# Kernel optimization log

Hardware: AMD Instinct MI355X
Metric: run time of the kernel (lower is better)

## Reference

```python
import jax, jax.numpy as jnp
import numpy as np

NU, NS, NM = 80000, 20000, 30000
D = 128
E_UI, E_MM = 1_500_000, 480_000
B, L = 2048, 32
LAYERS = 2


def spmm(rows, cols, vals, x, n):
    # sparse [n,n] @ dense [n,d] via gather + segment_sum
    return jax.ops.segment_sum(vals[:, None] * x[cols], rows, num_segments=n)


def setup_inputs() -> dict:
    key = jax.random.key(0)
    ks = jax.random.split(key, 20)
    inp = {}
    inp['mashup_inputs'] = jax.random.randint(ks[0], (B,), 0, NM, dtype=jnp.int32)
    inp['service_inputs'] = jax.random.randint(ks[1], (B,), 0, NS, dtype=jnp.int32)
    inp['member_masked'] = jax.random.randint(ks[2], (B, L), 0, NU, dtype=jnp.int32)
    # variable-length compose lists: length in [1, L]; mask==1 marks padding
    lens = jax.random.randint(ks[3], (B, 1), 1, L + 1)
    inp['mask'] = (jnp.arange(L)[None, :] >= lens).astype(jnp.float32)
    inp['member_masked'] = jnp.where(inp['mask'] > 0, 0, inp['member_masked'])
    inp['adj_rows'] = jax.random.randint(ks[4], (E_UI,), 0, NU + NS, dtype=jnp.int32)
    inp['adj_cols'] = jax.random.randint(ks[5], (E_UI,), 0, NU + NS, dtype=jnp.int32)
    inp['adj_vals'] = jax.random.uniform(ks[6], (E_UI,)) * 0.1
    inp['A_rows'] = jax.random.randint(ks[7], (E_MM,), 0, NM, dtype=jnp.int32)
    inp['A_cols'] = jax.random.randint(ks[8], (E_MM,), 0, NM, dtype=jnp.int32)
    inp['A_vals'] = jax.random.uniform(ks[9], (E_MM,)) * 0.1
    inp['d_inv'] = jax.random.uniform(ks[10], (NM,)) * 0.1
    s = 0.05
    inp['user_tbl'] = jax.random.normal(ks[11], (NU, D)) * s
    inp['service_tbl'] = jax.random.normal(ks[12], (NS, D)) * s
    inp['mashup_tbl'] = jax.random.normal(ks[13], (NM, D)) * s
    inp['att_w1'] = jax.random.normal(ks[14], (2 * D, 16)) * s
    inp['att_b1'] = jnp.zeros((16,))
    inp['att_w2'] = jax.random.normal(ks[15], (16, 1)) * s
    inp['att_b2'] = jnp.zeros((1,))
    inp['pred_w1'] = jax.random.normal(ks[16], (3 * D, 8)) * s
    inp['pred_b1'] = jnp.zeros((8,))
    inp['pred_w2'] = jax.random.normal(ks[17], (8, 1)) * s
    inp['pred_b2'] = jnp.zeros((1,))
    return inp


def reference(mashup_inputs, service_inputs, member_masked, adj_rows, adj_cols,
              A_rows, A_cols, mask, user_tbl, service_tbl, mashup_tbl,
              adj_vals, A_vals, d_inv, att_w1, att_b1, att_w2, att_b2,
              pred_w1, pred_b1, pred_w2, pred_b2):
    # HyperConv on concatenated user+service embeddings (layer-mean aggregation)
    ui = jnp.concatenate([user_tbl, service_tbl], axis=0)  # [NU+NS, D]
    acc, h = ui, ui
    for _ in range(LAYERS):
        h = spmm(adj_rows, adj_cols, adj_vals, h, NU + NS)
        acc = acc + h
    ui = acc / (LAYERS + 1)
    user_e, service_e = ui[:NU], ui[NU:]
    service_emb = service_e[service_inputs]  # [B, D]

    # HyperConv2 on mashup graph: emb <- D^-1 A emb per layer, layer-mean
    acc, m = mashup_tbl, mashup_tbl
    for _ in range(LAYERS):
        m = d_inv[:, None] * spmm(A_rows, A_cols, A_vals, m, NM)
        acc = acc + m
    mashup_embedding = acc / (LAYERS + 1)

    # ragged gather + masked attention pooling over compose members
    member_emb = user_e[member_masked]                      # [B, L, D]
    svc_exp = jnp.broadcast_to(service_emb[:, None, :], (B, L, D))
    at_emb = jnp.concatenate([member_emb, svc_exp], axis=2)  # [B, L, 2D]
    hdn = jax.nn.relu(at_emb @ att_w1 + att_b1)             # [B, L, 16]
    scores = (hdn @ att_w2 + att_b2)[..., 0]                 # [B, L]
    scores = jnp.where(mask > 0, -1e9, scores)               # mask padding
    at_wt = jax.nn.softmax(scores, axis=1)
    g_att = jnp.einsum('bl,bld->bd', at_wt, member_emb)      # [B, D]

    mashup_emb = g_att + mashup_embedding[mashup_inputs]
    elem = mashup_emb * service_emb
    new_emb = jnp.concatenate([elem, mashup_emb, service_emb], axis=1)  # [B, 3D]
    hp = jax.nn.relu(new_emb @ pred_w1 + pred_b1)
    y = jax.nn.sigmoid(hp @ pred_w2 + pred_b2)               # [B, 1]
    return y
```

## Files before the change

kernel.cpp:

```cpp
#include <hip/hip_runtime.h>
#include <climits>

#define NU_ 80000
#define NS_ 20000
#define NM_ 30000
#define UIN_ (NU_ + NS_)
#define DD 128
#define LL 32
#define RPB 64
#define NCH 256
#define NBUK_UI ((UIN_ + RPB - 1) / RPB)
#define NBUK_MM ((NM_  + RPB - 1) / RPB)

#define F8_SCALE 512.0f
#define F8_INV   (1.0f / 512.0f)

typedef unsigned int   uint32;
typedef unsigned short ushort_t;
typedef unsigned char  uchar_t;
typedef float f32x2 __attribute__((ext_vector_type(2)));

__device__ __forceinline__ float bflo(uint32 u) { return __uint_as_float(u << 16); }
__device__ __forceinline__ float bfhi(uint32 u) { return __uint_as_float(u & 0xffff0000u); }
__device__ __forceinline__ uint32 f2bf(float f) {
    uint32 u = __float_as_uint(f);
    return (u + 0x7fffu + ((u >> 16) & 1u)) >> 16;
}
__device__ __forceinline__ uint32 pack2bf(float lo, float hi) {
    return f2bf(lo) | (f2bf(hi) << 16);
}

__device__ __forceinline__ float dec1_f8(uint32 b) {
    uint32 em = b & 0x7fu;
    uint32 s  = (b & 0x80u) << 24;
    float vn = __uint_as_float(s | (((em >> 3) + 120u) << 23) | ((em & 7u) << 20));
    float vd = (float)(int)em * 0.001953125f;
    vd = (b & 0x80u) ? -vd : vd;
    return (em >= 8u) ? vn : vd;
}
__device__ __forceinline__ uint32 enc1_f8(float f) {
    uint32 u = __float_as_uint(f);
    uint32 s = (u >> 31) << 7;
    float a = fabsf(f);
    if (a >= 448.0f) return s | 0x7Eu;
    if (a < 0.015625f) {
        int m = (int)(a * 512.0f + 0.5f);
        return s | (uint32)m;
    }
    uint32 au = u & 0x7fffffffu;
    au += 0x7FFFFu + ((au >> 20) & 1u);
    uint32 em = (((au >> 23) - 120u) << 3) | ((au >> 20) & 7u);
    if (em >= 0x7Fu) em = 0x7Eu;
    return s | em;
}
__device__ __forceinline__ f32x2 dec2_f8(uint32 u) {
#if __has_builtin(__builtin_amdgcn_cvt_pk_f32_fp8)
    return __builtin_amdgcn_cvt_pk_f32_fp8(u, false);
#else
    f32x2 r; r.x = dec1_f8(u & 0xffu); r.y = dec1_f8((u >> 8) & 0xffu); return r;
#endif
}
__device__ __forceinline__ f32x2 dec2_f8_hi(uint32 u) {
#if __has_builtin(__builtin_amdgcn_cvt_pk_f32_fp8)
    return __builtin_amdgcn_cvt_pk_f32_fp8(u, true);
#else
    f32x2 r; r.x = dec1_f8((u >> 16) & 0xffu); r.y = dec1_f8(u >> 24); return r;
#endif
}
__device__ __forceinline__ uint32 pack2f8(float lo, float hi) {
#if __has_builtin(__builtin_amdgcn_cvt_pk_fp8_f32)
    return (uint32)__builtin_amdgcn_cvt_pk_fp8_f32(lo, hi, 0, false) & 0xFFFFu;
#else
    return enc1_f8(lo) | (enc1_f8(hi) << 8);
#endif
}

__global__ void convert_fused(const float* __restrict__ user_tbl,
                              const float* __restrict__ service_tbl,
                              const float* __restrict__ mashup_tbl,
                              uint32* __restrict__ ui_bf, ushort_t* __restrict__ ui_f8,
                              uint32* __restrict__ mash_bf, ushort_t* __restrict__ mash_f8) {
    const size_t P_UI = (size_t)UIN_ * 64;
    const size_t P_MM = (size_t)NM_ * 64;
    const size_t SPLIT = (size_t)NU_ * DD;
    size_t stride = (size_t)gridDim.x * blockDim.x;
    for (size_t i = (size_t)blockIdx.x * blockDim.x + threadIdx.x; i < P_UI + P_MM; i += stride) {
        if (i < P_UI) {
            size_t e = i * 2;
            const float* s = (e < SPLIT) ? (user_tbl + e) : (service_tbl + (e - SPLIT));
            float2 v = *reinterpret_cast<const float2*>(s);
            ui_bf[i] = pack2bf(v.x, v.y);
            ui_f8[i] = (ushort_t)pack2f8(v.x * F8_SCALE, v.y * F8_SCALE);
        } else {
            size_t j = i - P_UI;
            float2 v = *reinterpret_cast<const float2*>(mashup_tbl + j * 2);
            mash_bf[j] = pack2bf(v.x, v.y);
            mash_f8[j] = (ushort_t)pack2f8(v.x * F8_SCALE, v.y * F8_SCALE);
        }
    }
}

__global__ __launch_bounds__(1024) void hist_fused(
    const int* __restrict__ rows_ui, int E_ui, int csz_ui, int* __restrict__ h_ui,
    const int* __restrict__ rows_mm, int E_mm, int csz_mm, int* __restrict__ h_mm) {
    __shared__ int hist[NBUK_UI];
    const int* rows; int E, csz, nbuk, c; int* h;
    if ((int)blockIdx.x < NCH) { rows = rows_ui; E = E_ui; csz = csz_ui; h = h_ui; nbuk = NBUK_UI; c = blockIdx.x; }
    else                       { rows = rows_mm; E = E_mm; csz = csz_mm; h = h_mm; nbuk = NBUK_MM; c = blockIdx.x - NCH; }
    for (int i = threadIdx.x; i < nbuk; i += 1024) hist[i] = 0;
    __syncthreads();
    const int lo = c * csz, hi = min(lo + csz, E);
    int i = lo + threadIdx.x;
    for (; i + 3 * 1024 < hi; i += 4 * 1024) {
        int r0 = rows[i];
        int r1 = rows[i + 1024];
        int r2 = rows[i + 2048];
        int r3 = rows[i + 3072];
        atomicAdd(&hist[r0 >> 6], 1);
        atomicAdd(&hist[r1 >> 6], 1);
        atomicAdd(&hist[r2 >> 6], 1);
        atomicAdd(&hist[r3 >> 6], 1);
    }
    for (; i < hi; i += 1024) atomicAdd(&hist[rows[i] >> 6], 1);
    __syncthreads();
    for (int b = threadIdx.x; b < nbuk; b += 1024)
        h[b * NCH + c] = hist[b];
}

__global__ __launch_bounds__(256) void scan_blocksum_fused(
    const int* __restrict__ h_ui, int n_ui, int* __restrict__ bs_ui, int nb_ui,
    const int* __restrict__ h_mm, int n_mm, int* __restrict__ bs_mm) {
    __shared__ int red[256];
    const int* cnt; int n, b; int* bsum;
    if ((int)blockIdx.x < nb_ui) { cnt = h_ui; n = n_ui; bsum = bs_ui; b = blockIdx.x; }
    else                         { cnt = h_mm; n = n_mm; bsum = bs_mm; b = blockIdx.x - nb_ui; }
    int base = b * 1024 + threadIdx.x * 4;
    int s = 0;
    if (base + 3 < n) {
        int4 v = *reinterpret_cast<const int4*>(cnt + base);
        s = v.x + v.y + v.z + v.w;
    } else {
        for (int i = base; i < n && i < base + 4; ++i) s += cnt[i];
    }
    red[threadIdx.x] = s;
    __syncthreads();
    for (int off = 128; off >= 1; off >>= 1) {
        if (threadIdx.x < off) red[threadIdx.x] += red[threadIdx.x + off];
        __syncthreads();
    }
    if (threadIdx.x == 0) bsum[b] = red[0];
}

__global__ __launch_bounds__(256) void scan_final_fused(
    int* __restrict__ h_ui, int n_ui, const int* __restrict__ bs_ui, int nb_ui,
    int* __restrict__ s_ui,
    int* __restrict__ h_mm, int n_mm, const int* __restrict__ bs_mm,
    int* __restrict__ s_mm) {
    __shared__ int lds[256];
    __shared__ int blk_off_s;
    const int tid = threadIdx.x;
    int* cnt; int n, b; const int* bsum; int* row_ptr;
    if ((int)blockIdx.x < nb_ui) { cnt = h_ui; n = n_ui; bsum = bs_ui; row_ptr = s_ui; b = blockIdx.x; }
    else                         { cnt = h_mm; n = n_mm; bsum = bs_mm; row_ptr = s_mm; b = blockIdx.x - nb_ui; }

    int s = 0;
    for (int j = tid; j < b; j += 256) s += bsum[j];
    lds[tid] = s;
    __syncthreads();
    for (int off = 128; off >= 1; off >>= 1) {
        if (tid < off) lds[tid] += lds[tid + off];
        __syncthreads();
    }
    if (tid == 0) blk_off_s = lds[0];
    __syncthreads();
    const int blk_off = blk_off_s;

    int base = b * 1024 + tid * 4;
    int c0 = 0, c1 = 0, c2 = 0, c3 = 0;
    if (base + 3 < n) {
        int4 v = *reinterpret_cast<const int4*>(cnt + base);
        c0 = v.x; c1 = v.y; c2 = v.z; c3 = v.w;
    } else {
        if (base     < n) c0 = cnt[base];
        if (base + 1 < n) c1 = cnt[base + 1];
        if (base + 2 < n) c2 = cnt[base + 2];
        if (base + 3 < n) c3 = cnt[base + 3];
    }
    int tsum = c0 + c1 + c2 + c3;
    __syncthreads();
    lds[tid] = tsum;
    __syncthreads();
    for (int off = 1; off < 256; off <<= 1) {
        int v = (tid >= off) ? lds[tid - off] : 0;
        __syncthreads();
        lds[tid] += v;
        __syncthreads();
    }
    int p0 = blk_off + ((tid > 0) ? lds[tid - 1] : 0);
    int p1 = p0 + c0, p2 = p1 + c1, p3 = p2 + c2, p4 = p3 + c3;

    if (base     < n) { row_ptr[base]     = p0; if (base     == n - 1) row_ptr[n] = p1; }
    if (base + 1 < n) { row_ptr[base + 1] = p1; if (base + 1 == n - 1) row_ptr[n] = p2; }
    if (base + 2 < n) { row_ptr[base + 2] = p2; if (base + 2 == n - 1) row_ptr[n] = p3; }
    if (base + 3 < n) { row_ptr[base + 3] = p3; if (base + 3 == n - 1) row_ptr[n] = p4; }
}

__global__ __launch_bounds__(1024) void scatter_fused(
    const int* __restrict__ rows_ui, const int* __restrict__ cols_ui,
    const float* __restrict__ vals_ui, const int* __restrict__ s_ui,
    int E_ui, int csz_ui, uint2* __restrict__ cvA_ui,
    const int* __restrict__ rows_mm, const int* __restrict__ cols_mm,
    const float* __restrict__ vals_mm, const int* __restrict__ s_mm,
    int E_mm, int csz_mm, uint2* __restrict__ cvA_mm) {
    __shared__ int cur[NBUK_UI];
    const int *rows, *cols; const float* vals; const int* s;
    int E, csz, nbuk, c; uint2* cvA;
    if ((int)blockIdx.x < NCH) {
        rows = rows_ui; cols = cols_ui; vals = vals_ui; s = s_ui;
        E = E_ui; csz = csz_ui; nbuk = NBUK_UI; c = blockIdx.x; cvA = cvA_ui;
    } else {
        rows = rows_mm; cols = cols_mm; vals = vals_mm; s = s_mm;
        E = E_mm; csz = csz_mm; nbuk = NBUK_MM; c = blockIdx.x - NCH; cvA = cvA_mm;
    }
    for (int b = threadIdx.x; b < nbuk; b += 1024) cur[b] = s[b * NCH + c];
    __syncthreads();
    const int lo = c * csz, hi = min(lo + csz, E);
    int i = lo + threadIdx.x;
    for (; i + 3 * 1024 < hi; i += 4 * 1024) {
        int   r0 = rows[i],        r1 = rows[i + 1024];
        int   r2 = rows[i + 2048], r3 = rows[i + 3072];
        int   q0 = cols[i],        q1 = cols[i + 1024];
        int   q2 = cols[i + 2048], q3 = cols[i + 3072];
        float v0 = vals[i],        v1 = vals[i + 1024];
        float v2 = vals[i + 2048], v3 = vals[i + 3072];
        int p0 = atomicAdd(&cur[r0 >> 6], 1);
        int p1 = atomicAdd(&cur[r1 >> 6], 1);
        int p2 = atomicAdd(&cur[r2 >> 6], 1);
        int p3 = atomicAdd(&cur[r3 >> 6], 1);
        cvA[p0] = make_uint2((uint32)q0 | ((uint32)(r0 & 63) << 25), __float_as_uint(v0));
        cvA[p1] = make_uint2((uint32)q1 | ((uint32)(r1 & 63) << 25), __float_as_uint(v1));
        cvA[p2] = make_uint2((uint32)q2 | ((uint32)(r2 & 63) << 25), __float_as_uint(v2));
        cvA[p3] = make_uint2((uint32)q3 | ((uint32)(r3 & 63) << 25), __float_as_uint(v3));
    }
    for (; i < hi; i += 1024) {
        int r = rows[i];
        int pos = atomicAdd(&cur[r >> 6], 1);
        cvA[pos] = make_uint2((uint32)cols[i] | ((uint32)(r & 63) << 25),
                              __float_as_uint(vals[i]));
    }
}

__device__ __forceinline__ void sort_one_bucket(
    const uint2* __restrict__ cvA, const int* __restrict__ s,
    uint2* __restrict__ cvB, int* __restrict__ row_ptr, int nrows, int b,
    int* cnt, int* cur) {
    const int tid  = threadIdx.x;
    const int base = s[b * NCH];
    const int endb = s[(b + 1) * NCH];

    if (tid < RPB) cnt[tid] = 0;
    __syncthreads();
    for (int i = base + tid; i < endb; i += 256)
        atomicAdd(&cnt[cvA[i].x >> 25], 1);
    __syncthreads();
    if (tid < 64) {
        int c = cnt[tid];
        int x = c;
        #pragma unroll
        for (int off = 1; off < 64; off <<= 1) {
            int v = __shfl_up(x, off);
            if (tid >= off) x += v;
        }
        int excl = base + x - c;
        cur[tid] = excl;
        int grow = b * RPB + tid;
        if (grow <= nrows) row_ptr[grow] = excl;
    }
    __syncthreads();
    for (int i = base + tid; i < endb; i += 256) {
        uint2 e = cvA[i];
        int rl  = (int)(e.x >> 25);
        int pos = atomicAdd(&cur[rl], 1);
        cvB[pos] = make_uint2(e.x & 0x1FFFFFFu, e.y);
    }
}

__global__ __launch_bounds__(256) void sort_fused(
    const uint2* __restrict__ cvA_ui, const int* __restrict__ s_ui,
    uint2* __restrict__ cvB_ui, int* __restrict__ rp_ui,
    const uint2* __restrict__ cvA_mm, const int* __restrict__ s_mm,
    uint2* __restrict__ cvB_mm, int* __restrict__ rp_mm) {
    __shared__ int cnt[RPB];
    __shared__ int cur[RPB];
    if ((int)blockIdx.x < NBUK_UI)
        sort_one_bucket(cvA_ui, s_ui, cvB_ui, rp_ui, UIN_, blockIdx.x, cnt, cur);
    else
        sort_one_bucket(cvA_mm, s_mm, cvB_mm, rp_mm, NM_, blockIdx.x - NBUK_UI, cnt, cur);
}

template <int MODE>
__device__ __forceinline__ void pull_row(
    const int wid, const int lane,
    const int* __restrict__ row_ptr, const uint2* __restrict__ cv,
    const uchar_t* __restrict__ x, const float* __restrict__ d_inv,
    const uint32* __restrict__ orig_bf, const uchar_t* __restrict__ hprev_f8,
    void* __restrict__ out)
{
    const int q    = lane >> 4;
    const int ql   = lane & 15;
    const int beg  = row_ptr[wid];
    const int end  = row_ptr[wid + 1];
    const int boff = ql << 3;

    float a0 = 0.f, a1 = 0.f, a2 = 0.f, a3 = 0.f;
    float a4 = 0.f, a5 = 0.f, a6 = 0.f, a7 = 0.f;

    int e = beg + q;
    for (; e + 12 < end; e += 16) {
        uint2 p0 = cv[e],     p1 = cv[e + 4];
        uint2 p2 = cv[e + 8], p3 = cv[e + 12];
        uint2 g0 = *reinterpret_cast<const uint2*>(x + (((size_t)p0.x) << 7) + boff);
        uint2 g1 = *reinterpret_cast<const uint2*>(x + (((size_t)p1.x) << 7) + boff);
        uint2 g2 = *reinterpret_cast<const uint2*>(x + (((size_t)p2.x) << 7) + boff);
        uint2 g3 = *reinterpret_cast<const uint2*>(x + (((size_t)p3.x) << 7) + boff);
        float v0 = __uint_as_float(p0.y), v1 = __uint_as_float(p1.y);
        float v2 = __uint_as_float(p2.y), v3 = __uint_as_float(p3.y);
        {
            f32x2 d0 = dec2_f8(g0.x), d1 = dec2_f8_hi(g0.x);
            f32x2 d2 = dec2_f8(g0.y), d3 = dec2_f8_hi(g0.y);
            a0 += v0 * d0.x; a1 += v0 * d0.y; a2 += v0 * d1.x; a3 += v0 * d1.y;
            a4 += v0 * d2.x; a5 += v0 * d2.y; a6 += v0 * d3.x; a7 += v0 * d3.y;
        }
        {
            f32x2 d0 = dec2_f8(g1.x), d1 = dec2_f8_hi(g1.x);
            f32x2 d2 = dec2_f8(g1.y), d3 = dec2_f8_hi(g1.y);
            a0 += v1 * d0.x; a1 += v1 * d0.y; a2 += v1 * d1.x; a3 += v1 * d1.y;
            a4 += v1 * d2.x; a5 += v1 * d2.y; a6 += v1 * d3.x; a7 += v1 * d3.y;
        }
        {
            f32x2 d0 = dec2_f8(g2.x), d1 = dec2_f8_hi(g2.x);
            f32x2 d2 = dec2_f8(g2.y), d3 = dec2_f8_hi(g2.y);
            a0 += v2 * d0.x; a1 += v2 * d0.y; a2 += v2 * d1.x; a3 += v2 * d1.y;
            a4 += v2 * d2.x; a5 += v2 * d2.y; a6 += v2 * d3.x; a7 += v2 * d3.y;
        }
        {
            f32x2 d0 = dec2_f8(g3.x), d1 = dec2_f8_hi(g3.x);
            f32x2 d2 = dec2_f8(g3.y), d3 = dec2_f8_hi(g3.y);
            a0 += v3 * d0.x; a1 += v3 * d0.y; a2 += v3 * d1.x; a3 += v3 * d1.y;
            a4 += v3 * d2.x; a5 += v3 * d2.y; a6 += v3 * d3.x; a7 += v3 * d3.y;
        }
    }
    for (; e < end; e += 4) {
        uint2 pa = cv[e];
        uint2 ga = *reinterpret_cast<const uint2*>(x + (((size_t)pa.x) << 7) + boff);
        float va = __uint_as_float(pa.y);
        f32x2 d0 = dec2_f8(ga.x), d1 = dec2_f8_hi(ga.x);
        f32x2 d2 = dec2_f8(ga.y), d3 = dec2_f8_hi(ga.y);
        a0 += va * d0.x; a1 += va * d0.y; a2 += va * d1.x; a3 += va * d1.y;
        a4 += va * d2.x; a5 += va * d2.y; a6 += va * d3.x; a7 += va * d3.y;
    }

    a0 += __shfl_xor(a0, 16); a0 += __shfl_xor(a0, 32);
    a1 += __shfl_xor(a1, 16); a1 += __shfl_xor(a1, 32);
    a2 += __shfl_xor(a2, 16); a2 += __shfl_xor(a2, 32);
    a3 += __shfl_xor(a3, 16); a3 += __shfl_xor(a3, 32);
    a4 += __shfl_xor(a4, 16); a4 += __shfl_xor(a4, 32);
    a5 += __shfl_xor(a5, 16); a5 += __shfl_xor(a5, 32);
    a6 += __shfl_xor(a6, 16); a6 += __shfl_xor(a6, 32);
    a7 += __shfl_xor(a7, 16); a7 += __shfl_xor(a7, 32);

    if (lane < 16) {
        if (MODE & 1) {
            float s = d_inv[wid];
            a0 *= s; a1 *= s; a2 *= s; a3 *= s;
            a4 *= s; a5 *= s; a6 *= s; a7 *= s;
        }
        if (MODE & 2) {
            const float inv3 = 1.0f / 3.0f;
            uint4 o = *reinterpret_cast<const uint4*>(orig_bf + (size_t)wid * 64 + (ql << 2));
            uint2 hp = *reinterpret_cast<const uint2*>(hprev_f8 + (((size_t)wid) << 7) + boff);
            f32x2 h0 = dec2_f8(hp.x), h1 = dec2_f8_hi(hp.x);
            f32x2 h2 = dec2_f8(hp.y), h3 = dec2_f8_hi(hp.y);
            uint4 r;
            r.x = pack2bf((bflo(o.x) + (h0.x + a0) * F8_INV) * inv3,
                          (bfhi(o.x) + (h0.y + a1) * F8_INV) * inv3);
            r.y = pack2bf((bflo(o.y) + (h1.x + a2) * F8_INV) * inv3,
                          (bfhi(o.y) + (h1.y + a3) * F8_INV) * inv3);
            r.z = pack2bf((bflo(o.z) + (h2.x + a4) * F8_INV) * inv3,
                          (bfhi(o.z) + (h2.y + a5) * F8_INV) * inv3);
            r.w = pack2bf((bflo(o.w) + (h3.x + a6) * F8_INV) * inv3,
                          (bfhi(o.w) + (h3.y + a7) * F8_INV) * inv3);
            *reinterpret_cast<uint4*>(reinterpret_cast<uint32*>(out) + (size_t)wid * 64 + (ql << 2)) = r;
        } else {
            uint2 r;
            r.x = pack2f8(a0, a1) | (pack2f8(a2, a3) << 16);
            r.y = pack2f8(a4, a5) | (pack2f8(a6, a7) << 16);
            *reinterpret_cast<uint2*>((uchar_t*)out + (((size_t)wid) << 7) + boff) = r;
        }
    }
}

__global__ __launch_bounds__(256) void pull_L1_fused(
    const int* __restrict__ rp_ui, const uint2* __restrict__ cv_ui,
    const uchar_t* __restrict__ x_ui, uchar_t* __restrict__ out_ui,
    const int* __restrict__ rp_mm, const uint2* __restrict__ cv_mm,
    const uchar_t* __restrict__ x_mm, const float* __restrict__ d_inv,
    uchar_t* __restrict__ out_mm, int ui_blocks)
{
    const int lane = threadIdx.x & 63;
    const int w    = threadIdx.x >> 6;
    if ((int)blockIdx.x < ui_blocks) {
        int wid = blockIdx.x * 4 + w;
        if (wid < UIN_)
            pull_row<0>(wid, lane, rp_ui, cv_ui, x_ui, nullptr, nullptr, nullptr, out_ui);
    } else {
        int wid = (blockIdx.x - ui_blocks) * 4 + w;
        if (wid < NM_)
            pull_row<1>(wid, lane, rp_mm, cv_mm, x_mm, d_inv, nullptr, nullptr, out_mm);
    }
}

__global__ __launch_bounds__(256) void pull_L2_fused(
    const int* __restrict__ rp_ui, const uint2* __restrict__ cv_ui,
    const uchar_t* __restrict__ h1_f8, const uint32* __restrict__ ui_bf,
    uint32* __restrict__ h2,
    const int* __restrict__ rp_mm, const uint2* __restrict__ cv_mm,
    const uchar_t* __restrict__ m1_f8, const float* __restrict__ d_inv,
    const uint32* __restrict__ mash_bf, uint32* __restrict__ m2, int ui_blocks)
{
    const int lane = threadIdx.x & 63;
    const int w    = threadIdx.x >> 6;
    if ((int)blockIdx.x < ui_blocks) {
        int wid = blockIdx.x * 4 + w;
        if (wid < UIN_)
            pull_row<2>(wid, lane, rp_ui, cv_ui, h1_f8, nullptr, ui_bf, h1_f8, h2);
    } else {
        int wid = (blockIdx.x - ui_blocks) * 4 + w;
        if (wid < NM_)
            pull_row<3>(wid, lane, rp_mm, cv_mm, m1_f8, d_inv, mash_bf, m1_f8, m2);
    }
}

__global__ __launch_bounds__(512) void attn_pred_kernel(
    const int* __restrict__ mashup_inputs, const int* __restrict__ service_inputs,
    const int* __restrict__ member_masked, const float* __restrict__ mask,
    const uint32* __restrict__ ui_final, const uint32* __restrict__ mash_final,
    const float* __restrict__ att_w1, const float* __restrict__ att_b1,
    const float* __restrict__ att_w2, const float* __restrict__ att_b2,
    const float* __restrict__ pred_w1, const float* __restrict__ pred_b1,
    const float* __restrict__ pred_w2, const float* __restrict__ pred_b2,
    float* __restrict__ out)
{
    const int b   = blockIdx.x;
    const int tid = threadIdx.x;

    __shared__ float mem_lds[LL * 129];
    __shared__ float svc_lds[DD];
    __shared__ float mash_lds[DD];
    __shared__ float w1_lds[2 * DD * 16];
    __shared__ float hdnw_lds[LL * 16];
    __shared__ float wt_lds[LL];
    __shared__ float new_lds[3 * DD];
    __shared__ float hp_lds[8];
    __shared__ int   midx[LL];

    if (tid < LL) midx[tid] = member_masked[b * LL + tid];
    for (int i = tid; i < 2 * DD * 16; i += 512) w1_lds[i] = att_w1[i];
    if (tid < 64) {
        int sidx = service_inputs[b];
        uint32 u = ui_final[(size_t)(NU_ + sidx) * 64 + tid];
        svc_lds[tid * 2]     = bflo(u);
        svc_lds[tid * 2 + 1] = bfhi(u);
    } else if (tid >= 448) {
        int t  = tid - 448;
        int mi = mashup_inputs[b];
        uint32 u = mash_final[(size_t)mi * 64 + t];
        mash_lds[t * 2]     = bflo(u);
        mash_lds[t * 2 + 1] = bfhi(u);
    }
    __syncthreads();

    for (int i = tid; i < LL * 64; i += 512) {
        int l = i >> 6, dp = (i & 63) * 2;
        uint32 u = ui_final[(size_t)midx[l] * 64 + (i & 63)];
        mem_lds[l * 129 + dp]     = bflo(u);
        mem_lds[l * 129 + dp + 1] = bfhi(u);
    }
    __syncthreads();

    {
        int l = tid >> 4, j = tid & 15;
        float acc = att_b1[j];
        const float* m = &mem_lds[l * 129];
        #pragma unroll 4
        for (int k = 0; k < DD; ++k) acc += m[k] * w1_lds[k * 16 + j];
        #pragma unroll 4
        for (int k = 0; k < DD; ++k) acc += svc_lds[k] * w1_lds[(DD + k) * 16 + j];
        acc = fmaxf(acc, 0.0f);
        hdnw_lds[l * 16 + j] = acc * att_w2[j];
    }
    __syncthreads();

    if (tid < 64) {
        float s = -3.0e38f;
        if (tid < LL) {
            s = att_b2[0];
            for (int j = 0; j < 16; ++j) s += hdnw_lds[tid * 16 + j];
            if (mask[b * LL + tid] > 0.0f) s = -1.0e9f;
        }
        float mx = s;
        for (int off = 16; off >= 1; off >>= 1) mx = fmaxf(mx, __shfl_xor(mx, off));
        float ex = (tid < LL) ? __expf(s - mx) : 0.0f;
        float sum = ex;
        for (int off = 16; off >= 1; off >>= 1) sum += __shfl_xor(sum, off);
        if (tid < LL) wt_lds[tid] = ex / sum;
    }
    __syncthreads();

    if (tid < DD) {
        float g = 0.0f;
        #pragma unroll 4
        for (int l = 0; l < LL; ++l) g += wt_lds[l] * mem_lds[l * 129 + tid];
        float me = g + mash_lds[tid];
        float sv = svc_lds[tid];
        new_lds[tid]          = me * sv;
        new_lds[DD + tid]     = me;
        new_lds[2 * DD + tid] = sv;
    }
    __syncthreads();

    if (tid < 8) {
        float acc = pred_b1[tid];
        for (int k = 0; k < 3 * DD; ++k) acc += new_lds[k] * pred_w1[k * 8 + tid];
        acc = fmaxf(acc, 0.0f);
        hp_lds[tid] = acc * pred_w2[tid];
    }
    __syncthreads();

    if (tid == 0) {
        float z = pred_b2[0];
        for (int j = 0; j < 8; ++j) z += hp_lds[j];
        out[b] = 1.0f / (1.0f + __expf(-z));
    }
}

extern "C" void kernel_launch(void* const* d_in, const int* in_sizes, int n_in,
                              void* d_out, int out_size, void* d_ws, size_t ws_size,
                              hipStream_t stream) {
    const int*   mashup_inputs  = (const int*)  d_in[0];
    const int*   service_inputs = (const int*)  d_in[1];
    const int*   member_masked  = (const int*)  d_in[2];
    const float* mask           = (const float*)d_in[3];
    const int*   adj_rows       = (const int*)  d_in[4];
    const int*   adj_cols       = (const int*)  d_in[5];
    const float* adj_vals       = (const float*)d_in[6];
    const int*   A_rows         = (const int*)  d_in[7];
    const int*   A_cols         = (const int*)  d_in[8];
    const float* A_vals         = (const float*)d_in[9];
    const float* d_inv          = (const float*)d_in[10];
    const float* user_tbl       = (const float*)d_in[11];
    const float* service_tbl    = (const float*)d_in[12];
    const float* mashup_tbl     = (const float*)d_in[13];
    const float* att_w1         = (const float*)d_in[14];
    const float* att_b1         = (const float*)d_in[15];
    const float* att_w2         = (const float*)d_in[16];
    const float* att_b2         = (const float*)d_in[17];
    const float* pred_w1        = (const float*)d_in[18];
    const float* pred_b1        = (const float*)d_in[19];
    const float* pred_w2        = (const float*)d_in[20];
    const float* pred_b2        = (const float*)d_in[21];

    const int E_ui = in_sizes[4];
    const int E_mm = in_sizes[7];
    const int B    = in_sizes[0];

    const int N_UI2  = NBUK_UI * NCH;
    const int N_MM2  = NBUK_MM * NCH;
    const int NB_UI  = (N_UI2 + 1023) / 1024;
    const int NB_MM  = (N_MM2 + 1023) / 1024;
    const int csz_ui = (E_ui + NCH - 1) / NCH;
    const int csz_mm = (E_mm + NCH - 1) / NCH;

    uint2*   cvA_ui  = (uint2*)d_ws;
    uint2*   cvA_mm  = cvA_ui + E_ui;
    uint2*   cvB_ui  = cvA_mm + E_mm;
    uint2*   cvB_mm  = cvB_ui + E_ui;
    int*     h_ui    = (int*)(cvB_mm + E_mm);
    int*     s_ui    = h_ui + N_UI2;
    int*     h_mm    = s_ui + N_UI2 + 4;
    int*     s_mm    = h_mm + N_MM2;
    int*     bs_ui   = s_mm + N_MM2 + 4;
    int*     bs_mm   = bs_ui + 512;
    int*     rp_ui   = bs_mm + 128;
    int*     rp_mm   = rp_ui + UIN_ + 4;
    uint32*  ui_bf   = (uint32*)(rp_mm + NM_ + 4);
    uint32*  mash_bf = ui_bf + (size_t)UIN_ * 64;
    uint32*  h2      = mash_bf + (size_t)NM_ * 64;
    uint32*  m2      = h2 + (size_t)UIN_ * 64;
    uchar_t* ui_f8   = (uchar_t*)(m2 + (size_t)NM_ * 64);
    uchar_t* h1_f8   = ui_f8 + (size_t)UIN_ * DD;
    uchar_t* mash_f8 = h1_f8 + (size_t)UIN_ * DD;
    uchar_t* m1_f8   = mash_f8 + (size_t)NM_ * DD;

    convert_fused<<<2048, 256, 0, stream>>>(user_tbl, service_tbl, mashup_tbl,
                                            ui_bf, (ushort_t*)ui_f8,
                                            mash_bf, (ushort_t*)mash_f8);

    hist_fused<<<2 * NCH, 1024, 0, stream>>>(adj_rows, E_ui, csz_ui, h_ui,
                                             A_rows, E_mm, csz_mm, h_mm);
    scan_blocksum_fused<<<NB_UI + NB_MM, 256, 0, stream>>>(h_ui, N_UI2, bs_ui, NB_UI,
                                                           h_mm, N_MM2, bs_mm);
    scan_final_fused<<<NB_UI + NB_MM, 256, 0, stream>>>(h_ui, N_UI2, bs_ui, NB_UI, s_ui,
                                                        h_mm, N_MM2, bs_mm, s_mm);
    scatter_fused<<<2 * NCH, 1024, 0, stream>>>(
        adj_rows, adj_cols, adj_vals, s_ui, E_ui, csz_ui, cvA_ui,
        A_rows, A_cols, A_vals, s_mm, E_mm, csz_mm, cvA_mm);
    sort_fused<<<NBUK_UI + NBUK_MM, 256, 0, stream>>>(
        cvA_ui, s_ui, cvB_ui, rp_ui,
        cvA_mm, s_mm, cvB_mm, rp_mm);

    const int ui_blocks = (UIN_ + 3) / 4;
    const int mm_blocks = (NM_ + 3) / 4;
    pull_L1_fused<<<ui_blocks + mm_blocks, 256, 0, stream>>>(
        rp_ui, cvB_ui, ui_f8, h1_f8,
        rp_mm, cvB_mm, mash_f8, d_inv, m1_f8, ui_blocks);
    pull_L2_fused<<<ui_blocks + mm_blocks, 256, 0, stream>>>(
        rp_ui, cvB_ui, h1_f8, ui_bf, h2,
        rp_mm, cvB_mm, m1_f8, d_inv, mash_bf, m2, ui_blocks);

    attn_pred_kernel<<<B, 512, 0, stream>>>(
        mashup_inputs, service_inputs, member_masked, mask,
        h2, m2,
        att_w1, att_b1, att_w2, att_b2,
        pred_w1, pred_b1, pred_w2, pred_b2,
        (float*)d_out);
}
```

Measured before the change: 262.8 us.

## Use nontemporal loads/stores for streaming data and split fused pull kernels

Streaming reads and writes of edge arrays, packed column/value pairs and table conversions now use nontemporal load/store builtins, so single-use data does not pollute cache needed by the gathers. The pull inner loop drops its separate remainder loop in favour of a predicated 4-way unrolled loop. The fused UI/mashup pull kernels are split into four separate launches, adding launch overhead and removing the concurrency of the two graphs within one grid.

```diff
diff --git a/kernel.cpp b/kernel.cpp
--- a/kernel.cpp
+++ b/kernel.cpp
@@ -15,9 +15,10 @@
 #define F8_SCALE 512.0f
 #define F8_INV   (1.0f / 512.0f)
 
-typedef unsigned int   uint32;
-typedef unsigned short ushort_t;
-typedef unsigned char  uchar_t;
+typedef unsigned int       uint32;
+typedef unsigned short     ushort_t;
+typedef unsigned char      uchar_t;
+typedef unsigned long long u64;
 typedef float f32x2 __attribute__((ext_vector_type(2)));
 
 __device__ __forceinline__ float bflo(uint32 u) { return __uint_as_float(u << 16); }
@@ -29,6 +30,19 @@
 __device__ __forceinline__ uint32 pack2bf(float lo, float hi) {
     return f2bf(lo) | (f2bf(hi) << 16);
 }
+
+__device__ __forceinline__ u64 ntload_u64(const void* p) {
+    return __builtin_nontemporal_load((const u64*)p);
+}
+__device__ __forceinline__ uint2 ntload_u2(const uint2* p) {
+    u64 t = __builtin_nontemporal_load((const u64*)p);
+    return make_uint2((uint32)t, (uint32)(t >> 32));
+}
+__device__ __forceinline__ void ntstore_u2(uint2* p, uint2 v) {
+    __builtin_nontemporal_store(((u64)v.y << 32) | (u64)v.x, (u64*)p);
+}
+__device__ __forceinline__ int   ntload_i(const int* p)   { return __builtin_nontemporal_load(p); }
+__device__ __forceinline__ float ntload_f(const float* p) { return __builtin_nontemporal_load(p); }
 
 __device__ __forceinline__ float dec1_f8(uint32 b) {
     uint32 em = b & 0x7fu;
@@ -88,14 +102,16 @@
         if (i < P_UI) {
             size_t e = i * 2;
             const float* s = (e < SPLIT) ? (user_tbl + e) : (service_tbl + (e - SPLIT));
-            float2 v = *reinterpret_cast<const float2*>(s);
-            ui_bf[i] = pack2bf(v.x, v.y);
-            ui_f8[i] = (ushort_t)pack2f8(v.x * F8_SCALE, v.y * F8_SCALE);
+            u64 t = ntload_u64(s);
+            float lo = __uint_as_float((uint32)t), hi = __uint_as_float((uint32)(t >> 32));
+            ui_bf[i] = pack2bf(lo, hi);
+            ui_f8[i] = (ushort_t)pack2f8(lo * F8_SCALE, hi * F8_SCALE);
         } else {
             size_t j = i - P_UI;
-            float2 v = *reinterpret_cast<const float2*>(mashup_tbl + j * 2);
-            mash_bf[j] = pack2bf(v.x, v.y);
-            mash_f8[j] = (ushort_t)pack2f8(v.x * F8_SCALE, v.y * F8_SCALE);
+            u64 t = ntload_u64(mashup_tbl + j * 2);
+            float lo = __uint_as_float((uint32)t), hi = __uint_as_float((uint32)(t >> 32));
+            mash_bf[j] = pack2bf(lo, hi);
+            mash_f8[j] = (ushort_t)pack2f8(lo * F8_SCALE, hi * F8_SCALE);
         }
     }
 }
@@ -112,16 +128,16 @@
     const int lo = c * csz, hi = min(lo + csz, E);
     int i = lo + threadIdx.x;
     for (; i + 3 * 1024 < hi; i += 4 * 1024) {
-        int r0 = rows[i];
-        int r1 = rows[i + 1024];
-        int r2 = rows[i + 2048];
-        int r3 = rows[i + 3072];
+        int r0 = ntload_i(rows + i);
+        int r1 = ntload_i(rows + i + 1024);
+        int r2 = ntload_i(rows + i + 2048);
+        int r3 = ntload_i(rows + i + 3072);
         atomicAdd(&hist[r0 >> 6], 1);
         atomicAdd(&hist[r1 >> 6], 1);
         atomicAdd(&hist[r2 >> 6], 1);
         atomicAdd(&hist[r3 >> 6], 1);
     }
-    for (; i < hi; i += 1024) atomicAdd(&hist[rows[i] >> 6], 1);
+    for (; i < hi; i += 1024) atomicAdd(&hist[ntload_i(rows + i) >> 6], 1);
     __syncthreads();
     for (int b = threadIdx.x; b < nbuk; b += 1024)
         h[b * NCH + c] = hist[b];
@@ -227,26 +243,26 @@
     const int lo = c * csz, hi = min(lo + csz, E);
     int i = lo + threadIdx.x;
     for (; i + 3 * 1024 < hi; i += 4 * 1024) {
-        int   r0 = rows[i],        r1 = rows[i + 1024];
-        int   r2 = rows[i + 2048], r3 = rows[i + 3072];
-        int   q0 = cols[i],        q1 = cols[i + 1024];
-        int   q2 = cols[i + 2048], q3 = cols[i + 3072];
-        float v0 = vals[i],        v1 = vals[i + 1024];
-        float v2 = vals[i + 2048], v3 = vals[i + 3072];
+        int   r0 = ntload_i(rows + i),        r1 = ntload_i(rows + i + 1024);
+        int   r2 = ntload_i(rows + i + 2048), r3 = ntload_i(rows + i + 3072);
+        int   q0 = ntload_i(cols + i),        q1 = ntload_i(cols + i + 1024);
+        int   q2 = ntload_i(cols + i + 2048), q3 = ntload_i(cols + i + 3072);
+        float v0 = ntload_f(vals + i),        v1 = ntload_f(vals + i + 1024);
+        float v2 = ntload_f(vals + i + 2048), v3 = ntload_f(vals + i + 3072);
         int p0 = atomicAdd(&cur[r0 >> 6], 1);
         int p1 = atomicAdd(&cur[r1 >> 6], 1);
         int p2 = atomicAdd(&cur[r2 >> 6], 1);
         int p3 = atomicAdd(&cur[r3 >> 6], 1);
-        cvA[p0] = make_uint2((uint32)q0 | ((uint32)(r0 & 63) << 25), __float_as_uint(v0));
-        cvA[p1] = make_uint2((uint32)q1 | ((uint32)(r1 & 63) << 25), __float_as_uint(v1));
-        cvA[p2] = make_uint2((uint32)q2 | ((uint32)(r2 & 63) << 25), __float_as_uint(v2));
-        cvA[p3] = make_uint2((uint32)q3 | ((uint32)(r3 & 63) << 25), __float_as_uint(v3));
+        ntstore_u2(cvA + p0, make_uint2((uint32)q0 | ((uint32)(r0 & 63) << 25), __float_as_uint(v0)));
+        ntstore_u2(cvA + p1, make_uint2((uint32)q1 | ((uint32)(r1 & 63) << 25), __float_as_uint(v1)));
+        ntstore_u2(cvA + p2, make_uint2((uint32)q2 | ((uint32)(r2 & 63) << 25), __float_as_uint(v2)));
+        ntstore_u2(cvA + p3, make_uint2((uint32)q3 | ((uint32)(r3 & 63) << 25), __float_as_uint(v3)));
     }
     for (; i < hi; i += 1024) {
-        int r = rows[i];
+        int r = ntload_i(rows + i);
         int pos = atomicAdd(&cur[r >> 6], 1);
-        cvA[pos] = make_uint2((uint32)cols[i] | ((uint32)(r & 63) << 25),
-                              __float_as_uint(vals[i]));
+        ntstore_u2(cvA + pos, make_uint2((uint32)ntload_i(cols + i) | ((uint32)(r & 63) << 25),
+                                         __float_as_uint(ntload_f(vals + i))));
     }
 }
 
@@ -261,7 +277,7 @@
     if (tid < RPB) cnt[tid] = 0;
     __syncthreads();
     for (int i = base + tid; i < endb; i += 256)
-        atomicAdd(&cnt[cvA[i].x >> 25], 1);
+        atomicAdd(&cnt[ntload_u2(cvA + i).x >> 25], 1);
     __syncthreads();
     if (tid < 64) {
         int c = cnt[tid];
@@ -278,10 +294,10 @@
     }
     __syncthreads();
     for (int i = base + tid; i < endb; i += 256) {
-        uint2 e = cvA[i];
+        uint2 e = ntload_u2(cvA + i);
         int rl  = (int)(e.x >> 25);
         int pos = atomicAdd(&cur[rl], 1);
-        cvB[pos] = make_uint2(e.x & 0x1FFFFFFu, e.y);
+        ntstore_u2(cvB + pos, make_uint2(e.x & 0x1FFFFFFu, e.y));
     }
 }
 
@@ -315,14 +331,18 @@
     float a0 = 0.f, a1 = 0.f, a2 = 0.f, a3 = 0.f;
     float a4 = 0.f, a5 = 0.f, a6 = 0.f, a7 = 0.f;
 
-    int e = beg + q;
-    for (; e + 12 < end; e += 16) {
-        uint2 p0 = cv[e],     p1 = cv[e + 4];
-        uint2 p2 = cv[e + 8], p3 = cv[e + 12];
+    for (int e = beg + q; e < end; e += 16) {
+        const bool b1 = e + 4 < end, b2 = e + 8 < end, b3 = e + 12 < end;
+        uint2 p0 = ntload_u2(cv + e);
+        uint2 p1 = make_uint2(0u, 0u), p2 = make_uint2(0u, 0u), p3 = make_uint2(0u, 0u);
+        if (b1) p1 = ntload_u2(cv + e + 4);
+        if (b2) p2 = ntload_u2(cv + e + 8);
+        if (b3) p3 = ntload_u2(cv + e + 12);
         uint2 g0 = *reinterpret_cast<const uint2*>(x + (((size_t)p0.x) << 7) + boff);
-        uint2 g1 = *reinterpret_cast<const uint2*>(x + (((size_t)p1.x) << 7) + boff);
-        uint2 g2 = *reinterpret_cast<const uint2*>(x + (((size_t)p2.x) << 7) + boff);
-        uint2 g3 = *reinterpret_cast<const uint2*>(x + (((size_t)p3.x) << 7) + boff);
+        uint2 g1 = make_uint2(0u, 0u), g2 = make_uint2(0u, 0u), g3 = make_uint2(0u, 0u);
+        if (b1) g1 = *reinterpret_cast<const uint2*>(x + (((size_t)p1.x) << 7) + boff);
+        if (b2) g2 = *reinterpret_cast<const uint2*>(x + (((size_t)p2.x) << 7) + boff);
+        if (b3) g3 = *reinterpret_cast<const uint2*>(x + (((size_t)p3.x) << 7) + boff);
         float v0 = __uint_as_float(p0.y), v1 = __uint_as_float(p1.y);
         float v2 = __uint_as_float(p2.y), v3 = __uint_as_float(p3.y);
         {
@@ -349,15 +369,6 @@
             a0 += v3 * d0.x; a1 += v3 * d0.y; a2 += v3 * d1.x; a3 += v3 * d1.y;
             a4 += v3 * d2.x; a5 += v3 * d2.y; a6 += v3 * d3.x; a7 += v3 * d3.y;
         }
-    }
-    for (; e < end; e += 4) {
-        uint2 pa = cv[e];
-        uint2 ga = *reinterpret_cast<const uint2*>(x + (((size_t)pa.x) << 7) + boff);
-        float va = __uint_as_float(pa.y);
-        f32x2 d0 = dec2_f8(ga.x), d1 = dec2_f8_hi(ga.x);
-        f32x2 d2 = dec2_f8(ga.y), d3 = dec2_f8_hi(ga.y);
-        a0 += va * d0.x; a1 += va * d0.y; a2 += va * d1.x; a3 += va * d1.y;
-        a4 += va * d2.x; a5 += va * d2.y; a6 += va * d3.x; a7 += va * d3.y;
     }
 
     a0 += __shfl_xor(a0, 16); a0 += __shfl_xor(a0, 32);
@@ -377,19 +388,22 @@
         }
         if (MODE & 2) {
             const float inv3 = 1.0f / 3.0f;
-            uint4 o = *reinterpret_cast<const uint4*>(orig_bf + (size_t)wid * 64 + (ql << 2));
-            uint2 hp = *reinterpret_cast<const uint2*>(hprev_f8 + (((size_t)wid) << 7) + boff);
-            f32x2 h0 = dec2_f8(hp.x), h1 = dec2_f8_hi(hp.x);
-            f32x2 h2 = dec2_f8(hp.y), h3 = dec2_f8_hi(hp.y);
+            const u64* op = (const u64*)(orig_bf + (size_t)wid * 64 + (ql << 2));
+            u64 o01 = ntload_u64(op);
+            u64 o23 = ntload_u64(op + 1);
+            u64 hp64 = ntload_u64(hprev_f8 + (((size_t)wid) << 7) + boff);
+            uint32 hpx = (uint32)hp64, hpy = (uint32)(hp64 >> 32);
+            f32x2 h0 = dec2_f8(hpx), h1 = dec2_f8_hi(hpx);
+            f32x2 h2 = dec2_f8(hpy), h3 = dec2_f8_hi(hpy);
             uint4 r;
-            r.x = pack2bf((bflo(o.x) + (h0.x + a0) * F8_INV) * inv3,
-                          (bfhi(o.x) + (h0.y + a1) * F8_INV) * inv3);
-            r.y = pack2bf((bflo(o.y) + (h1.x + a2) * F8_INV) * inv3,
-                          (bfhi(o.y) + (h1.y + a3) * F8_INV) * inv3);
-            r.z = pack2bf((bflo(o.z) + (h2.x + a4) * F8_INV) * inv3,
-                          (bfhi(o.z) + (h2.y + a5) * F8_INV) * inv3);
-            r.w = pack2bf((bflo(o.w) + (h3.x + a6) * F8_INV) * inv3,
-                          (bfhi(o.w) + (h3.y + a7) * F8_INV) * inv3);
+            r.x = pack2bf((bflo((uint32)o01)         + (h0.x + a0) * F8_INV) * inv3,
+                          (bfhi((uint32)o01)         + (h0.y + a1) * F8_INV) * inv3);
+            r.y = pack2bf((bflo((uint32)(o01 >> 32)) + (h1.x + a2) * F8_INV) * inv3,
+                          (bfhi((uint32)(o01 >> 32)) + (h1.y + a3) * F8_INV) * inv3);
+            r.z = pack2bf((bflo((uint32)o23)         + (h2.x + a4) * F8_INV) * inv3,
+                          (bfhi((uint32)o23)         + (h2.y + a5) * F8_INV) * inv3);
+            r.w = pack2bf((bflo((uint32)(o23 >> 32)) + (h3.x + a6) * F8_INV) * inv3,
+                          (bfhi((uint32)(o23 >> 32)) + (h3.y + a7) * F8_INV) * inv3);
             *reinterpret_cast<uint4*>(reinterpret_cast<uint32*>(out) + (size_t)wid * 64 + (ql << 2)) = r;
         } else {
             uint2 r;
@@ -400,45 +414,36 @@
     }
 }
 
-__global__ __launch_bounds__(256) void pull_L1_fused(
-    const int* __restrict__ rp_ui, const uint2* __restrict__ cv_ui,
-    const uchar_t* __restrict__ x_ui, uchar_t* __restrict__ out_ui,
-    const int* __restrict__ rp_mm, const uint2* __restrict__ cv_mm,
-    const uchar_t* __restrict__ x_mm, const float* __restrict__ d_inv,
-    uchar_t* __restrict__ out_mm, int ui_blocks)
-{
+__global__ __launch_bounds__(256) void pull_ui_l1(
+    const int* __restrict__ rp, const uint2* __restrict__ cv,
+    const uchar_t* __restrict__ x, uchar_t* __restrict__ out) {
     const int lane = threadIdx.x & 63;
-    const int w    = threadIdx.x >> 6;
-    if ((int)blockIdx.x < ui_blocks) {
-        int wid = blockIdx.x * 4 + w;
-        if (wid < UIN_)
-            pull_row<0>(wid, lane, rp_ui, cv_ui, x_ui, nullptr, nullptr, nullptr, out_ui);
-    } else {
-        int wid = (blockIdx.x - ui_blocks) * 4 + w;
-        if (wid < NM_)
-            pull_row<1>(wid, lane, rp_mm, cv_mm, x_mm, d_inv, nullptr, nullptr, out_mm);
-    }
-}
-
-__global__ __launch_bounds__(256) void pull_L2_fused(
-    const int* __restrict__ rp_ui, const uint2* __restrict__ cv_ui,
-    const uchar_t* __restrict__ h1_f8, const uint32* __restrict__ ui_bf,
-    uint32* __restrict__ h2,
-    const int* __restrict__ rp_mm, const uint2* __restrict__ cv_mm,
-    const uchar_t* __restrict__ m1_f8, const float* __restrict__ d_inv,
-    const uint32* __restrict__ mash_bf, uint32* __restrict__ m2, int ui_blocks)
-{
+    int wid = blockIdx.x * 4 + (threadIdx.x >> 6);
+    if (wid < UIN_) pull_row<0>(wid, lane, rp, cv, x, nullptr, nullptr, nullptr, out);
+}
+__global__ __launch_bounds__(256) void pull_mm_l1(
+    const int* __restrict__ rp, const uint2* __restrict__ cv,
+    const uchar_t* __restrict__ x, const float* __restrict__ d_inv,
+    uchar_t* __restrict__ out) {
     const int lane = threadIdx.x & 63;
-    const int w    = threadIdx.x >> 6;
-    if ((int)blockIdx.x < ui_blocks) {
-        int wid = blockIdx.x * 4 + w;
-        if (wid < UIN_)
-            pull_row<2>(wid, lane, rp_ui, cv_ui, h1_f8, nullptr, ui_bf, h1_f8, h2);
-    } else {
-        int wid = (blockIdx.x - ui_blocks) * 4 + w;
-        if (wid < NM_)
-            pull_row<3>(wid, lane, rp_mm, cv_mm, m1_f8, d_inv, mash_bf, m1_f8, m2);
-    }
+    int wid = blockIdx.x * 4 + (threadIdx.x >> 6);
+    if (wid < NM_) pull_row<1>(wid, lane, rp, cv, x, d_inv, nullptr, nullptr, out);
+}
+__global__ __launch_bounds__(256) void pull_ui_l2(
+    const int* __restrict__ rp, const uint2* __restrict__ cv,
+    const uchar_t* __restrict__ h1, const uint32* __restrict__ orig_bf,
+    uint32* __restrict__ out) {
+    const int lane = threadIdx.x & 63;
+    int wid = blockIdx.x * 4 + (threadIdx.x >> 6);
+    if (wid < UIN_) pull_row<2>(wid, lane, rp, cv, h1, nullptr, orig_bf, h1, out);
+}
+__global__ __launch_bounds__(256) void pull_mm_l2(
+    const int* __restrict__ rp, const uint2* __restrict__ cv,
+    const uchar_t* __restrict__ m1, const float* __restrict__ d_inv,
+    const uint32* __restrict__ orig_bf, uint32* __restrict__ out) {
+    const int lane = threadIdx.x & 63;
+    int wid = blockIdx.x * 4 + (threadIdx.x >> 6);
+    if (wid < NM_) pull_row<3>(wid, lane, rp, cv, m1, d_inv, orig_bf, m1, out);
 }
 
 __global__ __launch_bounds__(512) void attn_pred_kernel(
@@ -621,12 +626,10 @@
 
     const int ui_blocks = (UIN_ + 3) / 4;
     const int mm_blocks = (NM_ + 3) / 4;
-    pull_L1_fused<<<ui_blocks + mm_blocks, 256, 0, stream>>>(
-        rp_ui, cvB_ui, ui_f8, h1_f8,
-        rp_mm, cvB_mm, mash_f8, d_inv, m1_f8, ui_blocks);
-    pull_L2_fused<<<ui_blocks + mm_blocks, 256, 0, stream>>>(
-        rp_ui, cvB_ui, h1_f8, ui_bf, h2,
-        rp_mm, cvB_mm, m1_f8, d_inv, mash_bf, m2, ui_blocks);
+    pull_mm_l1<<<mm_blocks, 256, 0, stream>>>(rp_mm, cvB_mm, mash_f8, d_inv, m1_f8);
+    pull_ui_l1<<<ui_blocks, 256, 0, stream>>>(rp_ui, cvB_ui, ui_f8, h1_f8);
+    pull_mm_l2<<<mm_blocks, 256, 0, stream>>>(rp_mm, cvB_mm, m1_f8, d_inv, mash_bf, m2);
+    pull_ui_l2<<<ui_blocks, 256, 0, stream>>>(rp_ui, cvB_ui, h1_f8, ui_bf, h2);
 
     attn_pred_kernel<<<B, 512, 0, stream>>>(
         mashup_inputs, service_inputs, member_masked, mask,
```

Result: slower. 343.0 us (+30.5%).
